# Performance work log

Hardware: AMD Instinct MI355X
Metric: run time of the kernel (lower is better)

The kernel has to match this reference:

```python
import jax, jax.numpy as jnp
import numpy as np

EMBED_DIM = 2048
NUM_HEADS = 16
B, L = 1, 4096


def setup_inputs() -> dict:
    key = jax.random.key(0)
    ks = jax.random.split(key, 6)
    s = 1.0 / np.sqrt(EMBED_DIM)
    return {
        "hidden_states": jax.random.normal(ks[0], (B, L, EMBED_DIM), jnp.float32),
        "Wq": jax.random.normal(ks[1], (EMBED_DIM, EMBED_DIM), jnp.float32) * s,
        "bq": jnp.zeros((EMBED_DIM,), jnp.float32),
        "Wk": jax.random.normal(ks[2], (EMBED_DIM, EMBED_DIM), jnp.float32) * s,
        "bk": jnp.zeros((EMBED_DIM,), jnp.float32),
        "Wv": jax.random.normal(ks[3], (EMBED_DIM, EMBED_DIM), jnp.float32) * s,
        "bv": jnp.zeros((EMBED_DIM,), jnp.float32),
        "Wo": jax.random.normal(ks[4], (EMBED_DIM, EMBED_DIM), jnp.float32) * s,
        "bo": jnp.zeros((EMBED_DIM,), jnp.float32),
        "is_causal": 1,
    }


def reference(hidden_states, Wq, bq, Wk, bk, Wv, bv, Wo, bo, is_causal):
    Bc, Lc, D = hidden_states.shape
    H = NUM_HEADS
    Dh = D // H
    scale = Dh ** (-0.5)

    def proj(W, b):
        # torch Linear: x @ W.T + b; reshape to [B, H, L, Dh]
        y = jnp.einsum('bld,ed->ble', hidden_states, W) + b
        return y.reshape(Bc, Lc, H, Dh).transpose(0, 2, 1, 3)

    q = proj(Wq, bq)
    k = proj(Wk, bk)
    v = proj(Wv, bv)

    scores = jnp.einsum('bhqd,bhkd->bhqk', q, k) * scale  # [B,H,L,L]
    if is_causal:
        causal = jnp.triu(jnp.ones((Lc, Lc), dtype=bool), k=1)
        scores = jnp.where(causal, -jnp.inf, scores)
    w = jax.nn.softmax(scores, axis=-1)
    attn = jnp.einsum('bhqk,bhkd->bhqd', w, v)
    attn = attn.transpose(0, 2, 1, 3).reshape(Bc, Lc, D)
    return jnp.einsum('bld,ed->ble', attn, Wo) + bo
```

## Files before the change

### kernel.cpp

```cpp
#include <hip/hip_runtime.h>
#include <hip/hip_bf16.h>

typedef unsigned short u16;
typedef unsigned int u32;
typedef __attribute__((ext_vector_type(8))) short short8;
typedef __attribute__((ext_vector_type(4))) float f32x4;

#define L 4096
#define DMODEL 2048
#define NHEADS 16
#define DHEAD 128
#define QSCALE (0.08838834764831845f * 1.44269504088896340f)

__device__ __forceinline__ u16 f2bf(float f){
  union { float f; unsigned int i; } v; v.f = f;
  unsigned int u = v.i;
  u += 0x7fffu + ((u >> 16) & 1u);
  return (u16)(u >> 16);
}

__device__ __forceinline__ u32 cvtpk(float lo, float hi){
  u32 d;
  asm("v_cvt_pk_bf16_f32 %0, %1, %2" : "=v"(d) : "v"(lo), "v"(hi));
  return d;
}

__global__ void cast_all_kernel(const float* __restrict__ X, u16* __restrict__ Xo,
                                const float* __restrict__ w0, const float* __restrict__ w1,
                                const float* __restrict__ w2, const float* __restrict__ w3,
                                u16* __restrict__ o0, u16* __restrict__ o1,
                                u16* __restrict__ o2, u16* __restrict__ o3){
  const int y = blockIdx.y;
  const float* in = (y == 0) ? X : (y == 1) ? w0 : (y == 2) ? w1 : (y == 3) ? w2 : w3;
  u16* out = (y == 0) ? Xo : (y == 1) ? o0 : (y == 2) ? o1 : (y == 3) ? o2 : o3;
  const int n = (y == 0) ? (L * DMODEL) : (DMODEL * DMODEL);
  int stride = gridDim.x * blockDim.x * 4;
  for (int j = (blockIdx.x * blockDim.x + threadIdx.x) * 4; j < n; j += stride){
    float4 f = *reinterpret_cast<const float4*>(in + j);
    ushort4 o;
    o.x = f2bf(f.x); o.y = f2bf(f.y); o.z = f2bf(f.z); o.w = f2bf(f.w);
    *reinterpret_cast<ushort4*>(out + j) = o;
  }
}

__device__ __forceinline__ void gl_lds16(void* lds, const void* g){
  __builtin_amdgcn_global_load_lds(
      (const __attribute__((address_space(1))) unsigned int*)g,
      (__attribute__((address_space(3))) unsigned int*)lds, 16, 0, 0);
}

#define GBUF 8192

template<int MODE>
__device__ __forceinline__ void gemm128(const u16* __restrict__ A, const u16* __restrict__ W,
                                        const float* __restrict__ bias, void* __restrict__ outp,
                                        float cscale, int bx, int by, u16* gsm){
  const int tid = threadIdx.x;
  const int wid = tid >> 6, lane = tid & 63;
  const int wm = wid >> 1, wn = wid & 1;
  const int g = lane >> 4, r = lane & 15;

  const int srow = tid >> 2;
  const int sc = ((tid & 3) * 16) ^ (((srow >> 1) & 3) << 4);
  const u16* Ag = A + ((size_t)(bx * 128) + srow) * DMODEL + (sc >> 1);
  const u16* Bg = W + ((size_t)(by * 128) + srow) * DMODEL + (sc >> 1);

  f32x4 acc[4][4];
  #pragma unroll
  for (int m = 0; m < 4; ++m)
    #pragma unroll
    for (int n = 0; n < 4; ++n) acc[m][n] = (f32x4){0,0,0,0};

  const int NK = DMODEL / 32;

  auto STAGE = [&](int b, int tk){
    char* ab = (char*)(gsm + b * GBUF);
    char* bb = (char*)(gsm + b * GBUF + 4096);
    const int ke = tk * 32;
    #pragma unroll
    for (int i = 0; i < 2; ++i)
      gl_lds16(ab + i * 4096 + tid * 16 - lane * 16 + lane * 16 - tid * 16 + tid * 16,
               (const char*)(Ag + (size_t)(i * 64) * DMODEL + ke));
    #pragma unroll
    for (int i = 0; i < 2; ++i)
      gl_lds16(bb + i * 4096 + tid * 16,
               (const char*)(Bg + (size_t)(i * 64) * DMODEL + ke));
  };

  STAGE(0, 0); STAGE(1, 1);

  int cur = 0;
  for (int t = 0; t < NK; ++t){
    if (t < NK - 1) asm volatile("s_waitcnt vmcnt(4)" ::: "memory");
    else            asm volatile("s_waitcnt vmcnt(0)" ::: "memory");
    __builtin_amdgcn_sched_barrier(0);
    __builtin_amdgcn_s_barrier();
    __builtin_amdgcn_sched_barrier(0);

    if (t + 2 < NK){
      int nb = cur + 2; if (nb >= 3) nb -= 3;
      STAGE(nb, t + 2);
    }

    const char* ab = (const char*)(gsm + cur * GBUF);
    const char* bb = (const char*)(gsm + cur * GBUF + 4096);

    short8 af[4], bf[4];
    #pragma unroll
    for (int mt = 0; mt < 4; ++mt){
      const int ar = wm * 64 + mt * 16 + r;
      af[mt] = *reinterpret_cast<const short8*>(
          ab + ar * 64 + ((g * 16) ^ (((ar >> 1) & 3) << 4)));
    }
    #pragma unroll
    for (int nt = 0; nt < 4; ++nt){
      const int br = wn * 64 + nt * 16 + r;
      bf[nt] = *reinterpret_cast<const short8*>(
          bb + br * 64 + ((g * 16) ^ (((br >> 1) & 3) << 4)));
    }

    __builtin_amdgcn_s_setprio(1);
    #pragma unroll
    for (int mt = 0; mt < 4; ++mt)
      #pragma unroll
      for (int nt = 0; nt < 4; ++nt)
        acc[mt][nt] = __builtin_amdgcn_mfma_f32_16x16x32_bf16(af[mt], bf[nt], acc[mt][nt], 0, 0, 0);
    __builtin_amdgcn_s_setprio(0);

    ++cur; if (cur == 3) cur = 0;
  }

  #pragma unroll
  for (int nt = 0; nt < 4; ++nt){
    const int col = by * 128 + wn * 64 + nt * 16 + r;
    const float bv = bias[col & (DMODEL - 1)];
    #pragma unroll
    for (int mt = 0; mt < 4; ++mt){
      #pragma unroll
      for (int qi = 0; qi < 4; ++qi){
        const int row = bx * 128 + wm * 64 + mt * 16 + g * 4 + qi;
        if (MODE == 0){
          ((u16*)outp)[(size_t)((col & (DMODEL-1)) >> 7) * (L * DHEAD) + (size_t)row * DHEAD + (col & 127)]
              = f2bf((acc[mt][nt][qi] + bv) * cscale);
        } else if (MODE == 1){
          ((u16*)outp)[(size_t)((col & (DMODEL-1)) >> 7) * (DHEAD * L) + (size_t)(col & 127) * L + row]
              = f2bf(acc[mt][nt][qi] + bv);
        } else {
          ((float*)outp)[(size_t)row * DMODEL + col] = acc[mt][nt][qi] + bv;
        }
      }
    }
  }
}

__global__ __launch_bounds__(256, 3) void gemm_qkv(const u16* __restrict__ A,
    const u16* __restrict__ Wq, const u16* __restrict__ Wk, const u16* __restrict__ Wv,
    const float* __restrict__ bq, const float* __restrict__ bk, const float* __restrict__ bv,
    u16* __restrict__ Qb, u16* __restrict__ Kb, u16* __restrict__ Vtb){
  extern __shared__ u16 gsm[];
  int id = blockIdx.x;
  int nid = (id & 7) * 192 + (id >> 3);
  int by = nid >> 5, bx = nid & 31;
  int sel = by >> 4, byl = by & 15;
  const u16* W      = (sel == 0) ? Wq : (sel == 1) ? Wk : Wv;
  const float* bias = (sel == 0) ? bq : (sel == 1) ? bk : bv;
  if (sel < 2)
    gemm128<0>(A, W, bias, (sel == 0) ? (void*)Qb : (void*)Kb,
               (sel == 0) ? QSCALE : 1.0f, bx, byl, gsm);
  else
    gemm128<1>(A, W, bias, (void*)Vtb, 1.0f, bx, byl, gsm);
}

__global__ __launch_bounds__(256, 3) void gemm_o(const u16* __restrict__ A, const u16* __restrict__ W,
                                                 const float* __restrict__ bias, float* __restrict__ outp){
  extern __shared__ u16 gsm[];
  int id = blockIdx.x;
  int nid = (id & 7) * 64 + (id >> 3);
  int by = nid >> 5, bx = nid & 31;
  gemm128<2>(A, W, bias, (void*)outp, 1.0f, bx, by, gsm);
}


__device__ __forceinline__ void stage_K64(u16* buf, const u16* Kh, int kv0, int wid, int lane){
  #pragma unroll
  for (int i = 0; i < 4; ++i){
    int ib = (wid * 4 + i) * 1024;
    int off = ib + lane * 16;
    int row = off >> 8;
    int c = off & 255;
    int sc = c ^ ((row & 7) << 4);
    gl_lds16((char*)buf + ib, (const char*)(Kh + (size_t)(kv0 + row) * DHEAD) + sc);
  }
}

__device__ __forceinline__ void stage_V64(u16* buf, const u16* Vh, int kv0, int wid, int lane){
  #pragma unroll
  for (int i = 0; i < 4; ++i){
    int ib = (wid * 4 + i) * 1024;
    int off = ib + lane * 16;
    int row = off >> 7;
    int c = off & 127;
    int sc = c ^ ((row & 7) << 4);
    gl_lds16((char*)buf + ib, (const char*)(Vh + (size_t)row * L + kv0) + sc);
  }
}

__device__ __forceinline__ void sm_R(f32x4 (&s)[4], float &l, bool dg, int qrow,
                                     int kv0, int g, u32 (&paw)[2][4]){
  if (dg){
    #pragma unroll
    for (int cb = 0; cb < 4; ++cb){
      int kvb = kv0 + cb * 16 + g * 4;
      #pragma unroll
      for (int e = 0; e < 4; ++e)
        if (kvb + e > qrow) s[cb][e] = -1e30f;
    }
  }
  float rs = 0.f;
  u32 pk[4][2];
  #pragma unroll
  for (int cb = 0; cb < 4; ++cb){
    float p0 = __builtin_amdgcn_exp2f(s[cb][0]);
    float p1 = __builtin_amdgcn_exp2f(s[cb][1]);
    float p2 = __builtin_amdgcn_exp2f(s[cb][2]);
    float p3 = __builtin_amdgcn_exp2f(s[cb][3]);
    rs += (p0 + p1) + (p2 + p3);
    pk[cb][0] = cvtpk(p0, p1);
    pk[cb][1] = cvtpk(p2, p3);
  }
  rs += __shfl_xor(rs, 16);
  rs += __shfl_xor(rs, 32);
  l += rs;
  #pragma unroll
  for (int ks = 0; ks < 2; ++ks){
    #pragma unroll
    for (int h = 0; h < 2; ++h){
      u32 a = pk[ks * 2][h], b = pk[ks * 2 + 1][h];
      asm volatile("v_permlane32_swap_b32 %0, %1" : "+v"(a), "+v"(b));
      asm volatile("v_permlane16_swap_b32 %0, %1" : "+v"(a), "+v"(b));
      paw[ks][h] = a;
      paw[ks][2 + h] = b;
    }
  }
}

__global__ __launch_bounds__(256, 2) void attn_kernel(const u16* __restrict__ Q, const u16* __restrict__ Km,
                                                      const u16* __restrict__ Vt, u16* __restrict__ Ob,
                                                      const int* __restrict__ is_causal_p){
  extern __shared__ u16 smem[];
  u16* Ks  = smem;
  u16* Vsm = smem + 16384;

  const int lane = threadIdx.x & 63, wid = threadIdx.x >> 6;
  const int g = lane >> 4, r = lane & 15;

  int lg = (blockIdx.x & 7) * 64 + (blockIdx.x >> 3);
  int head = lg >> 5;
  int raw = lg & 31;
  int j = (head & 1) ? (31 - raw) : raw;
  const int jA = j, jB = 63 - j;
  const int causal = *is_causal_p;
  const int nt = causal ? (jB + 1) : 64;

  const u16* Qh = Q  + (size_t)head * L * DHEAD;
  const u16* Kh = Km + (size_t)head * L * DHEAD;
  const u16* Vh = Vt + (size_t)head * DHEAD * L;

  const int rowA = 64 * jA + wid * 16;
  const int rowB = 64 * jB + wid * 16;

  short8 qf[2][4];
  #pragma unroll
  for (int kb = 0; kb < 4; ++kb){
    qf[0][kb] = *reinterpret_cast<const short8*>(&Qh[(size_t)(rowA + r) * DHEAD + kb * 32 + g * 8]);
    qf[1][kb] = *reinterpret_cast<const short8*>(&Qh[(size_t)(rowB + r) * DHEAD + kb * 32 + g * 8]);
  }

  f32x4 o[2][8];
  #pragma unroll
  for (int m = 0; m < 2; ++m)
    #pragma unroll
    for (int db = 0; db < 8; ++db) o[m][db] = (f32x4){0.f, 0.f, 0.f, 0.f};
  float lA = 0.f, lB = 0.f;

  stage_K64(Ks,  Kh, 0, wid, lane);
  stage_V64(Vsm, Vh, 0, wid, lane);

  for (int t = 0; t < nt; ++t){
    const int kv0 = t * 64;
    const bool actA = (!causal) || (t <= jA);
    const bool dgA = causal && (t == jA);
    const bool dgB = causal && (t == jB);

    asm volatile("s_waitcnt vmcnt(0)" ::: "memory");
    __builtin_amdgcn_sched_barrier(0);
    __builtin_amdgcn_s_barrier();
    __builtin_amdgcn_sched_barrier(0);

    if (t + 1 < nt){
      stage_K64(Ks  + ((t + 1) & 1) * 8192, Kh, kv0 + 64, wid, lane);
      stage_V64(Vsm + ((t + 1) & 1) * 8192, Vh, kv0 + 64, wid, lane);
    }

    const char* Kb = (const char*)(Ks  + (t & 1) * 8192);
    const char* Vb = (const char*)(Vsm + (t & 1) * 8192);

    f32x4 s[2][4];
    #pragma unroll
    for (int m = 0; m < 2; ++m)
      #pragma unroll
      for (int cb = 0; cb < 4; ++cb) s[m][cb] = (f32x4){-16.f, -16.f, -16.f, -16.f};
    __builtin_amdgcn_s_setprio(1);
    #pragma unroll
    for (int cb = 0; cb < 4; ++cb){
      const int rr = cb * 16 + r;
      short8 kf[4];
      #pragma unroll
      for (int kb = 0; kb < 4; ++kb)
        kf[kb] = *reinterpret_cast<const short8*>(
            Kb + rr * 256 + ((kb * 64 + g * 16) ^ ((rr & 7) << 4)));
      if (actA){
        #pragma unroll
        for (int kb = 0; kb < 4; ++kb)
          s[0][cb] = __builtin_amdgcn_mfma_f32_16x16x32_bf16(kf[kb], qf[0][kb], s[0][cb], 0, 0, 0);
      }
      #pragma unroll
      for (int kb = 0; kb < 4; ++kb)
        s[1][cb] = __builtin_amdgcn_mfma_f32_16x16x32_bf16(kf[kb], qf[1][kb], s[1][cb], 0, 0, 0);
    }
    __builtin_amdgcn_s_setprio(0);

    u32 pawA[2][4], pawB[2][4];
    if (actA) sm_R(s[0], lA, dgA, rowA + r, kv0, g, pawA);
    sm_R(s[1], lB, dgB, rowB + r, kv0, g, pawB);

    __builtin_amdgcn_s_setprio(1);
    #pragma unroll
    for (int st = 0; st < 2; ++st){
      union { u32 u[4]; short8 v; } pa0, pa1;
      #pragma unroll
      for (int w = 0; w < 4; ++w){ pa0.u[w] = pawA[st][w]; pa1.u[w] = pawB[st][w]; }
      #pragma unroll
      for (int db = 0; db < 8; ++db){
        const int rv = db * 16 + r;
        short8 vf = *reinterpret_cast<const short8*>(
            Vb + rv * 128 + (((st * 32 + g * 8) * 2) ^ ((rv & 7) << 4)));
        if (actA)
          o[0][db] = __builtin_amdgcn_mfma_f32_16x16x32_bf16(pa0.v, vf, o[0][db], 0, 0, 0);
        o[1][db] = __builtin_amdgcn_mfma_f32_16x16x32_bf16(pa1.v, vf, o[1][db], 0, 0, 0);
      }
    }
    __builtin_amdgcn_s_setprio(0);
  }

  #pragma unroll
  for (int m = 0; m < 2; ++m){
    const int rbase = m ? rowB : rowA;
    const float lv = m ? lB : lA;
    float lb[4];
    #pragma unroll
    for (int qi = 0; qi < 4; ++qi) lb[qi] = __shfl(lv, g * 4 + qi);
    #pragma unroll
    for (int db = 0; db < 8; ++db)
      #pragma unroll
      for (int qi = 0; qi < 4; ++qi){
        float val = o[m][db][qi] / lb[qi];
        int qrow = rbase + g * 4 + qi;
        Ob[(size_t)qrow * DMODEL + head * DHEAD + db * 16 + r] = f2bf(val);
      }
  }
}

extern "C" void kernel_launch(void* const* d_in, const int* in_sizes, int n_in,
                              void* d_out, int out_size, void* d_ws, size_t ws_size,
                              hipStream_t stream){
  const float* X  = (const float*)d_in[0];
  const float* Wq = (const float*)d_in[1];
  const float* bq = (const float*)d_in[2];
  const float* Wk = (const float*)d_in[3];
  const float* bk = (const float*)d_in[4];
  const float* Wv = (const float*)d_in[5];
  const float* bv = (const float*)d_in[6];
  const float* Wo = (const float*)d_in[7];
  const float* bo = (const float*)d_in[8];
  const int*   isc = (const int*)d_in[9];

  char* ws = (char*)d_ws;
  u16* Xb  = (u16*)(ws);
  u16* Qb  = (u16*)(ws + 16777216);
  u16* Kb  = (u16*)(ws + 33554432);
  u16* Vtb = (u16*)(ws + 50331648);
  u16* Wqb = (u16*)(ws + 67108864);
  u16* Wkb = (u16*)(ws + 75497472);
  u16* Wvb = (u16*)(ws + 83886080);
  u16* Wob = (u16*)(ws + 92274688);
  u16* Ob  = Xb;

  (void)hipFuncSetAttribute(reinterpret_cast<const void*>(attn_kernel),
                            hipFuncAttributeMaxDynamicSharedMemorySize, 65536);
  (void)hipFuncSetAttribute(reinterpret_cast<const void*>(gemm_qkv),
                            hipFuncAttributeMaxDynamicSharedMemorySize, 49152);
  (void)hipFuncSetAttribute(reinterpret_cast<const void*>(gemm_o),
                            hipFuncAttributeMaxDynamicSharedMemorySize, 49152);

  cast_all_kernel<<<dim3(1024, 5), 256, 0, stream>>>(X, Xb, Wq, Wk, Wv, Wo,
                                                     Wqb, Wkb, Wvb, Wob);

  gemm_qkv<<<1536, 256, 49152, stream>>>(Xb, Wqb, Wkb, Wvb, bq, bk, bv, Qb, Kb, Vtb);

  attn_kernel<<<512, 256, 65536, stream>>>(Qb, Kb, Vtb, Ob, isc);

  gemm_o<<<512, 256, 49152, stream>>>(Ob, Wob, bo, (float*)d_out);
}
```

Before: 309.3 us.

## Enlarge GEMM tiles to 256x128 with 512-thread blocks

The QKV and output-projection GEMMs now use 256x128 output tiles computed by 8 waves, up from 128x128 tiles with 4 waves. Each B tile staged in LDS now feeds twice as many rows, cutting weight re-reads, and per-stage loads drop from four to three. The swizzled block-id rasterization is replaced with a plain 2D grid, which may reduce L2 locality. The triple-buffered LDS grows to 72KB per block, and the new launch bounds may tighten the register budget enough to cause spills.

```diff
diff --git a/kernel.cpp b/kernel.cpp
--- a/kernel.cpp
+++ b/kernel.cpp
@@ -49,12 +49,12 @@
       (__attribute__((address_space(3))) unsigned int*)lds, 16, 0, 0);
 }
 
-#define GBUF 8192
+#define GBUF 12288
 
 template<int MODE>
-__device__ __forceinline__ void gemm128(const u16* __restrict__ A, const u16* __restrict__ W,
-                                        const float* __restrict__ bias, void* __restrict__ outp,
-                                        float cscale, int bx, int by, u16* gsm){
+__device__ __forceinline__ void gemm_core(const u16* __restrict__ A, const u16* __restrict__ W,
+                                          const float* __restrict__ bias, void* __restrict__ outp,
+                                          float cscale, int bx, int by, u16* gsm){
   const int tid = threadIdx.x;
   const int wid = tid >> 6, lane = tid & 63;
   const int wm = wid >> 1, wn = wid & 1;
@@ -62,8 +62,9 @@
 
   const int srow = tid >> 2;
   const int sc = ((tid & 3) * 16) ^ (((srow >> 1) & 3) << 4);
-  const u16* Ag = A + ((size_t)(bx * 128) + srow) * DMODEL + (sc >> 1);
+  const u16* Ag = A + ((size_t)(bx * 256) + srow) * DMODEL + (sc >> 1);
   const u16* Bg = W + ((size_t)(by * 128) + srow) * DMODEL + (sc >> 1);
+  const int ldsw = wid * 1024;
 
   f32x4 acc[4][4];
   #pragma unroll
@@ -75,23 +76,18 @@
 
   auto STAGE = [&](int b, int tk){
     char* ab = (char*)(gsm + b * GBUF);
-    char* bb = (char*)(gsm + b * GBUF + 4096);
+    char* bb = (char*)(gsm + b * GBUF + 8192);
     const int ke = tk * 32;
-    #pragma unroll
-    for (int i = 0; i < 2; ++i)
-      gl_lds16(ab + i * 4096 + tid * 16 - lane * 16 + lane * 16 - tid * 16 + tid * 16,
-               (const char*)(Ag + (size_t)(i * 64) * DMODEL + ke));
-    #pragma unroll
-    for (int i = 0; i < 2; ++i)
-      gl_lds16(bb + i * 4096 + tid * 16,
-               (const char*)(Bg + (size_t)(i * 64) * DMODEL + ke));
+    gl_lds16(ab + ldsw,        (const char*)(Ag + ke));
+    gl_lds16(ab + 8192 + ldsw, (const char*)(Ag + (size_t)128 * DMODEL + ke));
+    gl_lds16(bb + ldsw,        (const char*)(Bg + ke));
   };
 
   STAGE(0, 0); STAGE(1, 1);
 
   int cur = 0;
   for (int t = 0; t < NK; ++t){
-    if (t < NK - 1) asm volatile("s_waitcnt vmcnt(4)" ::: "memory");
+    if (t < NK - 1) asm volatile("s_waitcnt vmcnt(3)" ::: "memory");
     else            asm volatile("s_waitcnt vmcnt(0)" ::: "memory");
     __builtin_amdgcn_sched_barrier(0);
     __builtin_amdgcn_s_barrier();
@@ -103,7 +99,7 @@
     }
 
     const char* ab = (const char*)(gsm + cur * GBUF);
-    const char* bb = (const char*)(gsm + cur * GBUF + 4096);
+    const char* bb = (const char*)(gsm + cur * GBUF + 8192);
 
     short8 af[4], bf[4];
     #pragma unroll
@@ -133,17 +129,17 @@
   #pragma unroll
   for (int nt = 0; nt < 4; ++nt){
     const int col = by * 128 + wn * 64 + nt * 16 + r;
-    const float bv = bias[col & (DMODEL - 1)];
+    const float bv = bias[col];
     #pragma unroll
     for (int mt = 0; mt < 4; ++mt){
       #pragma unroll
       for (int qi = 0; qi < 4; ++qi){
-        const int row = bx * 128 + wm * 64 + mt * 16 + g * 4 + qi;
+        const int row = bx * 256 + wm * 64 + mt * 16 + g * 4 + qi;
         if (MODE == 0){
-          ((u16*)outp)[(size_t)((col & (DMODEL-1)) >> 7) * (L * DHEAD) + (size_t)row * DHEAD + (col & 127)]
+          ((u16*)outp)[(size_t)(col >> 7) * (L * DHEAD) + (size_t)row * DHEAD + (col & 127)]
               = f2bf((acc[mt][nt][qi] + bv) * cscale);
         } else if (MODE == 1){
-          ((u16*)outp)[(size_t)((col & (DMODEL-1)) >> 7) * (DHEAD * L) + (size_t)(col & 127) * L + row]
+          ((u16*)outp)[(size_t)(col >> 7) * (DHEAD * L) + (size_t)(col & 127) * L + row]
               = f2bf(acc[mt][nt][qi] + bv);
         } else {
           ((float*)outp)[(size_t)row * DMODEL + col] = acc[mt][nt][qi] + bv;
@@ -153,31 +149,26 @@
   }
 }
 
-__global__ __launch_bounds__(256, 3) void gemm_qkv(const u16* __restrict__ A,
+__global__ __launch_bounds__(512, 4) void gemm_qkv(const u16* __restrict__ A,
     const u16* __restrict__ Wq, const u16* __restrict__ Wk, const u16* __restrict__ Wv,
     const float* __restrict__ bq, const float* __restrict__ bk, const float* __restrict__ bv,
     u16* __restrict__ Qb, u16* __restrict__ Kb, u16* __restrict__ Vtb){
   extern __shared__ u16 gsm[];
-  int id = blockIdx.x;
-  int nid = (id & 7) * 192 + (id >> 3);
-  int by = nid >> 5, bx = nid & 31;
-  int sel = by >> 4, byl = by & 15;
+  const int sel = blockIdx.y >> 4;
+  const int byl = blockIdx.y & 15;
   const u16* W      = (sel == 0) ? Wq : (sel == 1) ? Wk : Wv;
   const float* bias = (sel == 0) ? bq : (sel == 1) ? bk : bv;
   if (sel < 2)
-    gemm128<0>(A, W, bias, (sel == 0) ? (void*)Qb : (void*)Kb,
-               (sel == 0) ? QSCALE : 1.0f, bx, byl, gsm);
+    gemm_core<0>(A, W, bias, (sel == 0) ? (void*)Qb : (void*)Kb,
+                 (sel == 0) ? QSCALE : 1.0f, blockIdx.x, byl, gsm);
   else
-    gemm128<1>(A, W, bias, (void*)Vtb, 1.0f, bx, byl, gsm);
-}
-
-__global__ __launch_bounds__(256, 3) void gemm_o(const u16* __restrict__ A, const u16* __restrict__ W,
+    gemm_core<1>(A, W, bias, (void*)Vtb, 1.0f, blockIdx.x, byl, gsm);
+}
+
+__global__ __launch_bounds__(512, 4) void gemm_o(const u16* __restrict__ A, const u16* __restrict__ W,
                                                  const float* __restrict__ bias, float* __restrict__ outp){
   extern __shared__ u16 gsm[];
-  int id = blockIdx.x;
-  int nid = (id & 7) * 64 + (id >> 3);
-  int by = nid >> 5, bx = nid & 31;
-  gemm128<2>(A, W, bias, (void*)outp, 1.0f, bx, by, gsm);
+  gemm_core<2>(A, W, bias, (void*)outp, 1.0f, blockIdx.x, blockIdx.y, gsm);
 }
 
 
@@ -399,16 +390,16 @@
   (void)hipFuncSetAttribute(reinterpret_cast<const void*>(attn_kernel),
                             hipFuncAttributeMaxDynamicSharedMemorySize, 65536);
   (void)hipFuncSetAttribute(reinterpret_cast<const void*>(gemm_qkv),
-                            hipFuncAttributeMaxDynamicSharedMemorySize, 49152);
+                            hipFuncAttributeMaxDynamicSharedMemorySize, 73728);
   (void)hipFuncSetAttribute(reinterpret_cast<const void*>(gemm_o),
-                            hipFuncAttributeMaxDynamicSharedMemorySize, 49152);
+                            hipFuncAttributeMaxDynamicSharedMemorySize, 73728);
 
   cast_all_kernel<<<dim3(1024, 5), 256, 0, stream>>>(X, Xb, Wq, Wk, Wv, Wo,
                                                      Wqb, Wkb, Wvb, Wob);
 
-  gemm_qkv<<<1536, 256, 49152, stream>>>(Xb, Wqb, Wkb, Wvb, bq, bk, bv, Qb, Kb, Vtb);
+  gemm_qkv<<<dim3(16, 48), 512, 73728, stream>>>(Xb, Wqb, Wkb, Wvb, bq, bk, bv, Qb, Kb, Vtb);
 
   attn_kernel<<<512, 256, 65536, stream>>>(Qb, Kb, Vtb, Ob, isc);
 
-  gemm_o<<<512, 256, 49152, stream>>>(Ob, Wob, bo, (float*)d_out);
-}
+  gemm_o<<<dim3(16, 16), 512, 73728, stream>>>(Ob, Wob, bo, (float*)d_out);
+}
```

After: 282.4 us. -8.7%, faster.
